# Performance work log

Measured on AMD Instinct MI355X. Metric: run time of the kernel, lower is better.

## Reference

```python
import jax, jax.numpy as jnp
import numpy as np

D = 512
H = 8
DV = D // H  # 64
NEG_INF = -1e30


def setup_inputs() -> dict:
    key = jax.random.key(0)
    ks = jax.random.split(key, 10)
    B, S = 4, 2048
    x = jax.random.normal(ks[0], (B, D, S), dtype=jnp.float32)
    mask = jnp.ones((B, S), dtype=jnp.float32)
    s = 1.0 / np.sqrt(D)
    sv = 1.0 / np.sqrt(D)
    # per-head Linear(d -> dv) weights stacked: [H, dv, d] (torch Linear layout W @ x)
    Wq = jax.random.uniform(ks[1], (H, DV, D), jnp.float32, -s, s)
    bq = jax.random.uniform(ks[2], (H, DV), jnp.float32, -s, s)
    Wk = jax.random.uniform(ks[3], (H, DV, D), jnp.float32, -s, s)
    bk = jax.random.uniform(ks[4], (H, DV), jnp.float32, -s, s)
    Wv = jax.random.uniform(ks[5], (H, DV, D), jnp.float32, -s, s)
    bv = jax.random.uniform(ks[6], (H, DV), jnp.float32, -s, s)
    W0 = jax.random.uniform(ks[7], (D, D), jnp.float32, -sv, sv)
    b0 = jax.random.uniform(ks[8], (D,), jnp.float32, -sv, sv)
    return {"x": x, "mask": mask, "Wq": Wq, "bq": bq, "Wk": Wk, "bk": bk,
            "Wv": Wv, "bv": bv, "W0": W0, "b0": b0}


def reference(x, mask, Wq, bq, Wk, bk, Wv, bv, W0, b0):
    # x: [B, d, S] -> xt: [B, S, d]
    xt = jnp.transpose(x, (0, 2, 1))
    # fused per-head projections: [B, H, S, dv]
    q = jnp.einsum('bsd,hed->bhse', xt, Wq) + bq[None, :, None, :]
    k = jnp.einsum('bsd,hed->bhse', xt, Wk) + bk[None, :, None, :]
    v = jnp.einsum('bsd,hed->bhse', xt, Wv) + bv[None, :, None, :]
    dv = q.shape[-1]
    scores = jnp.einsum('bhse,bhte->bhst', q, k) * (1.0 / np.sqrt(dv))
    # mask_logits (QANet style): keep where mask==1, else -1e30; mask over key dim
    h_mask = mask[:, None, None, :]  # [B,1,1,S]
    scores = scores * h_mask + (1.0 - h_mask) * NEG_INF
    p = jax.nn.softmax(scores, axis=-1)
    # zero out fully-masked query rows via v_mask on query dim
    p = p * mask[:, None, :, None]
    out = jnp.einsum('bhst,bhte->bhse', p, v)  # [B,H,S,dv]
    # concat heads along feature dim -> [B, S, d]
    B, _, S, _ = out.shape
    heads = jnp.transpose(out, (0, 2, 1, 3)).reshape(B, S, -1)
    y = heads @ W0.T + b0  # output projection
    return jnp.transpose(y, (0, 2, 1))  # [B, d, S]
```

## Files before the change

### kernel.cpp

```cpp
#include <hip/hip_runtime.h>

#define B_  4
#define D_  512
#define H_  8
#define DV_ 64
#define S_  2048

typedef __bf16 bf16;
typedef bf16  bf16x8 __attribute__((ext_vector_type(8)));
typedef bf16  bf16x4 __attribute__((ext_vector_type(4)));
typedef float f32x4  __attribute__((ext_vector_type(4)));

#define MFMA(a, b, c) __builtin_amdgcn_mfma_f32_16x16x32_bf16((a), (b), (c), 0, 0, 0)

#define GLOAD_LDS(g, l)                                                     \
    __builtin_amdgcn_global_load_lds(                                       \
        (const __attribute__((address_space(1))) void*)(g),                 \
        (__attribute__((address_space(3))) void*)(l), 16, 0, 0)

__global__ __launch_bounds__(256) void prep(
    const float* __restrict__ x, const float* __restrict__ Wq,
    const float* __restrict__ Wk, const float* __restrict__ Wv,
    const float* __restrict__ W0, bf16* __restrict__ xb, bf16* __restrict__ Wb) {
    const int bid = blockIdx.x;
    if (bid < 4096) {
        __shared__ float tile[32][33];
        const int sblk = bid % 64;
        const int dblk = (bid / 64) % 16;
        const int b    = bid / 1024;
        const int d0 = dblk * 32, s0 = sblk * 32;
        const int tx = threadIdx.x & 31;
        const int ty = threadIdx.x >> 5;
        const float* xp = x + (size_t)b * D_ * S_;
#pragma unroll
        for (int i = 0; i < 32; i += 8)
            tile[ty + i][tx] = xp[(size_t)(d0 + ty + i) * S_ + s0 + tx];
        __syncthreads();
        bf16* xbp = xb + ((size_t)b * S_ + s0) * D_ + d0;
#pragma unroll
        for (int i = 0; i < 32; i += 8)
            xbp[(size_t)(ty + i) * D_ + tx] = (bf16)tile[tx][ty + i];
    } else {
        const int f0 = ((bid - 4096) * 256 + threadIdx.x) * 16;
        const int src = f0 >> 18;
        const int off = f0 & 262143;
        const float* W = (src == 0) ? Wq : (src == 1) ? Wk : (src == 2) ? Wv : W0;
        float4 v0 = *(const float4*)&W[off];
        float4 v1 = *(const float4*)&W[off + 4];
        float4 v2 = *(const float4*)&W[off + 8];
        float4 v3 = *(const float4*)&W[off + 12];
        bf16x8 h0 = {(bf16)v0.x, (bf16)v0.y, (bf16)v0.z, (bf16)v0.w,
                     (bf16)v1.x, (bf16)v1.y, (bf16)v1.z, (bf16)v1.w};
        bf16x8 h1 = {(bf16)v2.x, (bf16)v2.y, (bf16)v2.z, (bf16)v2.w,
                     (bf16)v3.x, (bf16)v3.y, (bf16)v3.z, (bf16)v3.w};
        *(bf16x8*)&Wb[f0]     = h0;
        *(bf16x8*)&Wb[f0 + 8] = h1;
    }
}

__global__ __launch_bounds__(256) void gemm_qkv(
    const bf16* __restrict__ A, const bf16* __restrict__ Wb,
    const float* __restrict__ bq, const float* __restrict__ bk,
    const float* __restrict__ bv,
    bf16* __restrict__ Q, bf16* __restrict__ K, bf16* __restrict__ Vt) {
    __shared__ bf16 Asl[8192];
    __shared__ bf16 Bsl[8192];

    const int tid = threadIdx.x;
    const int w = tid >> 6, lane = tid & 63;
    const int m16 = lane & 15, quad = lane >> 4;
    const int wr = w & 1, wc = w >> 1;

    const int nblk = blockIdx.x % 12;
    const int mblk = blockIdx.x / 12;
    const int m0 = mblk * 128, n0 = nblk * 128;

    f32x4 acc[4][4];
#pragma unroll
    for (int i = 0; i < 4; ++i)
#pragma unroll
        for (int j = 0; j < 4; ++j) acc[i][j] = (f32x4){0.f, 0.f, 0.f, 0.f};

    for (int k0 = 0; k0 < D_; k0 += 64) {
        __syncthreads();
#pragma unroll
        for (int i = 0; i < 4; ++i) {
            const int c  = w * 4 + i;
            const int mt = c >> 1, kk = c & 1;
            const int row = mt * 16 + m16;
            const int col = k0 + kk * 32 + quad * 8;
            GLOAD_LDS(&A[(size_t)(m0 + row) * D_ + col],  &Asl[(c * 64 + lane) * 8]);
            GLOAD_LDS(&Wb[(size_t)(n0 + row) * D_ + col], &Bsl[(c * 64 + lane) * 8]);
        }
        __syncthreads();
#pragma unroll
        for (int kk = 0; kk < 2; ++kk) {
            bf16x8 af[4], bfv[4];
#pragma unroll
            for (int t = 0; t < 4; ++t) {
                af[t]  = *(const bf16x8*)&Asl[(((wr * 4 + t) * 2 + kk) * 64 + lane) * 8];
                bfv[t] = *(const bf16x8*)&Bsl[(((wc * 4 + t) * 2 + kk) * 64 + lane) * 8];
            }
#pragma unroll
            for (int mt = 0; mt < 4; ++mt)
#pragma unroll
                for (int nt = 0; nt < 4; ++nt)
                    acc[mt][nt] = MFMA(af[mt], bfv[nt], acc[mt][nt]);
        }
    }

    const int proj = n0 >> 9;
    const float* bias = (proj == 0) ? bq : (proj == 1) ? bk : bv;
#pragma unroll
    for (int mt = 0; mt < 4; ++mt)
#pragma unroll
        for (int nt = 0; nt < 4; ++nt) {
            const int nlin = n0 + wc * 64 + nt * 16 + m16;
            const int nr = nlin & 511;
            const int h = nr >> 6, e = nr & 63;
            const float bia = bias[nr];
            const int srow = m0 + wr * 64 + mt * 16 + quad * 4;
            const int b = srow >> 11, s = srow & 2047;
            if (proj == 2) {
                bf16x4 hv;
#pragma unroll
                for (int r = 0; r < 4; ++r) hv[r] = (bf16)(acc[mt][nt][r] + bia);
                *(bf16x4*)&Vt[(((size_t)b * H_ + h) * DV_ + e) * S_ + s] = hv;
            } else {
                bf16* dst = (proj == 0) ? Q : K;
#pragma unroll
                for (int r = 0; r < 4; ++r)
                    dst[(((size_t)b * H_ + h) * S_ + s + r) * DV_ + e] =
                        (bf16)(acc[mt][nt][r] + bia);
            }
        }
}

#define RS 36
__global__ __launch_bounds__(256, 2) void flash_attn(
    const bf16* __restrict__ Q, const bf16* __restrict__ K, const bf16* __restrict__ Vt,
    const float* __restrict__ mask, bf16* __restrict__ heads) {
    __shared__ union SMem {
        bf16 Ps[4][64][RS];
        struct { float O[64][65]; float L[64]; } red;
    } sm;

    const int bidx = blockIdx.x;
    const int qblk = bidx & 31;
    const int h    = (bidx >> 5) & 7;
    const int b    = bidx >> 8;
    const int q0   = qblk * 64;

    const int tid = threadIdx.x;
    const int w = tid >> 6, lane = tid & 63;
    const int m16 = lane & 15, quad = lane >> 4;

    const bf16* Qp = Q  + ((size_t)b * H_ + h) * S_ * DV_;
    const bf16* Kp = K  + ((size_t)b * H_ + h) * S_ * DV_;
    const bf16* Vp = Vt + ((size_t)b * H_ + h) * DV_ * S_;
    const float* mp = mask + (size_t)b * S_;

    bf16x8 qf[4][2];
#pragma unroll
    for (int mt = 0; mt < 4; ++mt)
#pragma unroll
        for (int kk = 0; kk < 2; ++kk) {
            bf16x8 v = *(const bf16x8*)&Qp[(size_t)(q0 + mt * 16 + m16) * DV_ +
                                           kk * 32 + quad * 8];
#pragma unroll
            for (int i = 0; i < 8; ++i) v[i] = (bf16)((float)v[i] * 0.125f);
            qf[mt][kk] = v;
        }

    bf16x8 ones;
#pragma unroll
    for (int i = 0; i < 8; ++i) ones[i] = (bf16)1.0f;

    f32x4 o[4][4];
    f32x4 lacc[4];
#pragma unroll
    for (int mt = 0; mt < 4; ++mt)
#pragma unroll
        for (int nt = 0; nt < 4; ++nt) o[mt][nt] = (f32x4){0.f, 0.f, 0.f, 0.f};
#pragma unroll
    for (int nt = 0; nt < 4; ++nt) lacc[nt] = (f32x4){0.f, 0.f, 0.f, 0.f};

    bf16x8 kfc[2][2], vfc[4];
    {
        const int tw = w * 32;
#pragma unroll
        for (int nt = 0; nt < 2; ++nt)
#pragma unroll
            for (int kk = 0; kk < 2; ++kk)
                kfc[nt][kk] = *(const bf16x8*)&Kp[(size_t)(tw + nt * 16 + m16) * DV_ +
                                                  kk * 32 + quad * 8];
#pragma unroll
        for (int mt = 0; mt < 4; ++mt)
            vfc[mt] = *(const bf16x8*)&Vp[(size_t)(mt * 16 + m16) * S_ + tw + quad * 8];
    }

    for (int t0 = 0; t0 < S_; t0 += 128) {
        const int tw = t0 + w * 32;
        const bool more = (t0 + 128) < S_;

        bf16x8 kfn[2][2], vfn[4];
        if (more) {
            const int twn = tw + 128;
#pragma unroll
            for (int nt = 0; nt < 2; ++nt)
#pragma unroll
                for (int kk = 0; kk < 2; ++kk)
                    kfn[nt][kk] = *(const bf16x8*)&Kp[(size_t)(twn + nt * 16 + m16) * DV_ +
                                                      kk * 32 + quad * 8];
#pragma unroll
            for (int mt = 0; mt < 4; ++mt)
                vfn[mt] = *(const bf16x8*)&Vp[(size_t)(mt * 16 + m16) * S_ + twn + quad * 8];
        }

        f32x4 sc[4][2];
#pragma unroll
        for (int mt = 0; mt < 4; ++mt)
#pragma unroll
            for (int nt = 0; nt < 2; ++nt) sc[mt][nt] = (f32x4){0.f, 0.f, 0.f, 0.f};
#pragma unroll
        for (int kk = 0; kk < 2; ++kk)
#pragma unroll
            for (int mt = 0; mt < 4; ++mt)
#pragma unroll
                for (int nt = 0; nt < 2; ++nt)
                    sc[mt][nt] = MFMA(qf[mt][kk], kfc[nt][kk], sc[mt][nt]);

        const float mk0 = mp[tw + m16],          mk1 = mp[tw + 16 + m16];
        const float ng0 = (1.0f - mk0) * -1e30f, ng1 = (1.0f - mk1) * -1e30f;
#pragma unroll
        for (int mt = 0; mt < 4; ++mt)
#pragma unroll
            for (int r = 0; r < 4; ++r) {
                const int row = mt * 16 + quad * 4 + r;
                sm.Ps[w][row][m16]      = (bf16)__expf(sc[mt][0][r] * mk0 + ng0);
                sm.Ps[w][row][16 + m16] = (bf16)__expf(sc[mt][1][r] * mk1 + ng1);
            }

        bf16x8 pf[4];
#pragma unroll
        for (int nt = 0; nt < 4; ++nt)
            pf[nt] = *(const bf16x8*)&sm.Ps[w][nt * 16 + m16][quad * 8];
#pragma unroll
        for (int mt = 0; mt < 4; ++mt)
#pragma unroll
            for (int nt = 0; nt < 4; ++nt) o[mt][nt] = MFMA(vfc[mt], pf[nt], o[mt][nt]);
#pragma unroll
        for (int nt = 0; nt < 4; ++nt) lacc[nt] = MFMA(ones, pf[nt], lacc[nt]);

        if (more) {
#pragma unroll
            for (int nt = 0; nt < 2; ++nt)
#pragma unroll
                for (int kk = 0; kk < 2; ++kk) kfc[nt][kk] = kfn[nt][kk];
#pragma unroll
            for (int mt = 0; mt < 4; ++mt) vfc[mt] = vfn[mt];
        }
    }

    __syncthreads();
#pragma unroll
    for (int ww = 0; ww < 4; ++ww) {
        if (w == ww) {
#pragma unroll
            for (int mt = 0; mt < 4; ++mt)
#pragma unroll
                for (int nt = 0; nt < 4; ++nt)
#pragma unroll
                    for (int r = 0; r < 4; ++r) {
                        float* slot = &sm.red.O[mt * 16 + quad * 4 + r][nt * 16 + m16];
                        *slot = (ww == 0) ? o[mt][nt][r] : (*slot + o[mt][nt][r]);
                    }
            if (quad == 0)
#pragma unroll
                for (int nt = 0; nt < 4; ++nt) {
                    float* ls = &sm.red.L[nt * 16 + m16];
                    *ls = (ww == 0) ? lacc[nt][0] : (*ls + lacc[nt][0]);
                }
        }
        __syncthreads();
    }

    const int ql = tid >> 2, ec = (tid & 3) * 16;
    const float l  = sm.red.L[ql];
    const float qm = mp[q0 + ql];
    const float inv = qm / l;
    bf16x8 hv[2];
#pragma unroll
    for (int c = 0; c < 2; ++c)
#pragma unroll
        for (int i = 0; i < 8; ++i)
            hv[c][i] = (bf16)(sm.red.O[ec + c * 8 + i][ql] * inv);
    bf16* dst = &heads[((size_t)b * S_ + q0 + ql) * D_ + h * DV_ + ec];
    *(bf16x8*)(dst)     = hv[0];
    *(bf16x8*)(dst + 8) = hv[1];
}

__global__ __launch_bounds__(256) void gemm_out(
    const bf16* __restrict__ A, const bf16* __restrict__ Wb,
    const float* __restrict__ b0, float* __restrict__ outp) {
    __shared__ bf16 Asl[8192];
    __shared__ bf16 Bsl[8192];

    const int tid = threadIdx.x;
    const int w = tid >> 6, lane = tid & 63;
    const int m16 = lane & 15, quad = lane >> 4;
    const int wr = w & 1, wc = w >> 1;

    const int nblk = blockIdx.x & 3;
    const int mblk = blockIdx.x >> 2;
    const int m0 = mblk * 128, n0 = nblk * 128;

    f32x4 acc[4][4];
#pragma unroll
    for (int i = 0; i < 4; ++i)
#pragma unroll
        for (int j = 0; j < 4; ++j) acc[i][j] = (f32x4){0.f, 0.f, 0.f, 0.f};

    for (int k0 = 0; k0 < D_; k0 += 64) {
        __syncthreads();
#pragma unroll
        for (int i = 0; i < 4; ++i) {
            const int c  = w * 4 + i;
            const int mt = c >> 1, kk = c & 1;
            const int row = mt * 16 + m16;
            const int col = k0 + kk * 32 + quad * 8;
            GLOAD_LDS(&A[(size_t)(m0 + row) * D_ + col], &Asl[(c * 64 + lane) * 8]);
            GLOAD_LDS(&Wb[(size_t)(1536 + n0 + row) * D_ + col], &Bsl[(c * 64 + lane) * 8]);
        }
        __syncthreads();
#pragma unroll
        for (int kk = 0; kk < 2; ++kk) {
            bf16x8 af[4], bfv[4];
#pragma unroll
            for (int t = 0; t < 4; ++t) {
                af[t]  = *(const bf16x8*)&Asl[(((wr * 4 + t) * 2 + kk) * 64 + lane) * 8];
                bfv[t] = *(const bf16x8*)&Bsl[(((wc * 4 + t) * 2 + kk) * 64 + lane) * 8];
            }
#pragma unroll
            for (int mt = 0; mt < 4; ++mt)
#pragma unroll
                for (int nt = 0; nt < 4; ++nt)
                    acc[mt][nt] = MFMA(af[mt], bfv[nt], acc[mt][nt]);
        }
    }

#pragma unroll
    for (int mt = 0; mt < 4; ++mt)
#pragma unroll
        for (int nt = 0; nt < 4; ++nt) {
            const int n = n0 + wc * 64 + nt * 16 + m16;
            const float bia = b0[n];
            const int srow = m0 + wr * 64 + mt * 16 + quad * 4;
            const int b = srow >> 11, s = srow & 2047;
            float4 vv;
            vv.x = acc[mt][nt][0] + bia;
            vv.y = acc[mt][nt][1] + bia;
            vv.z = acc[mt][nt][2] + bia;
            vv.w = acc[mt][nt][3] + bia;
            *(float4*)&outp[((size_t)b * D_ + n) * S_ + s] = vv;
        }
}

extern "C" void kernel_launch(void* const* d_in, const int* in_sizes, int n_in,
                              void* d_out, int out_size, void* d_ws, size_t ws_size,
                              hipStream_t stream) {
    const float* x    = (const float*)d_in[0];
    const float* mask = (const float*)d_in[1];
    const float* Wq   = (const float*)d_in[2];
    const float* bq   = (const float*)d_in[3];
    const float* Wk   = (const float*)d_in[4];
    const float* bk   = (const float*)d_in[5];
    const float* Wv   = (const float*)d_in[6];
    const float* bv   = (const float*)d_in[7];
    const float* W0   = (const float*)d_in[8];
    const float* b0   = (const float*)d_in[9];
    float* out = (float*)d_out;

    char* ws = (char*)d_ws;
    const size_t SEG = (size_t)B_ * S_ * D_ * sizeof(bf16);
    bf16* xb    = (bf16*)(ws);
    bf16* Qb    = (bf16*)(ws + SEG);
    bf16* Kb    = (bf16*)(ws + 2 * SEG);
    bf16* Vt    = (bf16*)(ws + 3 * SEG);
    bf16* Wb    = (bf16*)(ws + 4 * SEG);
    bf16* heads = xb;

    prep<<<dim3(4096 + 256), dim3(256), 0, stream>>>(x, Wq, Wk, Wv, W0, xb, Wb);
    gemm_qkv<<<dim3(64 * 12), dim3(256), 0, stream>>>(xb, Wb, bq, bk, bv, Qb, Kb, Vt);
    flash_attn<<<dim3(B_ * H_ * (S_ / 64)), dim3(256), 0, stream>>>(Qb, Kb, Vt, mask, heads);
    gemm_out<<<dim3(64 * 4), dim3(256), 0, stream>>>(heads, Wb, b0, out);
}
```

Before: 216.1 us.

## Compute transposed scores so P stays in registers, dropping LDS round-trip

Computes S^T = K·Q^T so each lane's MFMA accumulator already matches the B-operand layout needed for the P·V MFMA, removing the per-iteration LDS write and read of the probability tile. V fragments are gathered as two 4-element loads in a matching permuted key order, and the mask is loaded as vectors. The explicit register double-buffering of the next K/V tile is also removed, which frees registers but exposes global load latency unless the compiler or occupancy hides it.

```diff
diff --git a/kernel.cpp b/kernel.cpp
--- a/kernel.cpp
+++ b/kernel.cpp
@@ -136,14 +136,10 @@
         }
 }
 
-#define RS 36
 __global__ __launch_bounds__(256, 2) void flash_attn(
     const bf16* __restrict__ Q, const bf16* __restrict__ K, const bf16* __restrict__ Vt,
     const float* __restrict__ mask, bf16* __restrict__ heads) {
-    __shared__ union SMem {
-        bf16 Ps[4][64][RS];
-        struct { float O[64][65]; float L[64]; } red;
-    } sm;
+    __shared__ struct { float O[64][65]; float L[64]; } red;
 
     const int bidx = blockIdx.x;
     const int qblk = bidx & 31;
@@ -162,14 +158,14 @@
 
     bf16x8 qf[4][2];
 #pragma unroll
-    for (int mt = 0; mt < 4; ++mt)
+    for (int qt = 0; qt < 4; ++qt)
 #pragma unroll
         for (int kk = 0; kk < 2; ++kk) {
-            bf16x8 v = *(const bf16x8*)&Qp[(size_t)(q0 + mt * 16 + m16) * DV_ +
+            bf16x8 v = *(const bf16x8*)&Qp[(size_t)(q0 + qt * 16 + m16) * DV_ +
                                            kk * 32 + quad * 8];
 #pragma unroll
             for (int i = 0; i < 8; ++i) v[i] = (bf16)((float)v[i] * 0.125f);
-            qf[mt][kk] = v;
+            qf[qt][kk] = v;
         }
 
     bf16x8 ones;
@@ -181,85 +177,66 @@
 #pragma unroll
     for (int mt = 0; mt < 4; ++mt)
 #pragma unroll
-        for (int nt = 0; nt < 4; ++nt) o[mt][nt] = (f32x4){0.f, 0.f, 0.f, 0.f};
-#pragma unroll
-    for (int nt = 0; nt < 4; ++nt) lacc[nt] = (f32x4){0.f, 0.f, 0.f, 0.f};
-
-    bf16x8 kfc[2][2], vfc[4];
-    {
-        const int tw = w * 32;
-#pragma unroll
-        for (int nt = 0; nt < 2; ++nt)
-#pragma unroll
-            for (int kk = 0; kk < 2; ++kk)
-                kfc[nt][kk] = *(const bf16x8*)&Kp[(size_t)(tw + nt * 16 + m16) * DV_ +
-                                                  kk * 32 + quad * 8];
-#pragma unroll
-        for (int mt = 0; mt < 4; ++mt)
-            vfc[mt] = *(const bf16x8*)&Vp[(size_t)(mt * 16 + m16) * S_ + tw + quad * 8];
-    }
+        for (int qt = 0; qt < 4; ++qt) o[mt][qt] = (f32x4){0.f, 0.f, 0.f, 0.f};
+#pragma unroll
+    for (int qt = 0; qt < 4; ++qt) lacc[qt] = (f32x4){0.f, 0.f, 0.f, 0.f};
 
     for (int t0 = 0; t0 < S_; t0 += 128) {
         const int tw = t0 + w * 32;
-        const bool more = (t0 + 128) < S_;
-
-        bf16x8 kfn[2][2], vfn[4];
-        if (more) {
-            const int twn = tw + 128;
-#pragma unroll
-            for (int nt = 0; nt < 2; ++nt)
-#pragma unroll
-                for (int kk = 0; kk < 2; ++kk)
-                    kfn[nt][kk] = *(const bf16x8*)&Kp[(size_t)(twn + nt * 16 + m16) * DV_ +
-                                                      kk * 32 + quad * 8];
-#pragma unroll
-            for (int mt = 0; mt < 4; ++mt)
-                vfn[mt] = *(const bf16x8*)&Vp[(size_t)(mt * 16 + m16) * S_ + twn + quad * 8];
-        }
-
-        f32x4 sc[4][2];
+
+        bf16x8 kf[2][2];
+#pragma unroll
+        for (int tt = 0; tt < 2; ++tt)
+#pragma unroll
+            for (int kk = 0; kk < 2; ++kk)
+                kf[tt][kk] = *(const bf16x8*)&Kp[(size_t)(tw + tt * 16 + m16) * DV_ +
+                                                 kk * 32 + quad * 8];
+        bf16x8 vf[4];
+#pragma unroll
+        for (int mt = 0; mt < 4; ++mt) {
+            const bf16* vb = &Vp[(size_t)(mt * 16 + m16) * S_ + tw + quad * 4];
+            const bf16x4 lo = *(const bf16x4*)vb;
+            const bf16x4 hi = *(const bf16x4*)(vb + 16);
+#pragma unroll
+            for (int i = 0; i < 4; ++i) { vf[mt][i] = lo[i]; vf[mt][4 + i] = hi[i]; }
+        }
+        const f32x4 mq0 = *(const f32x4*)&mp[tw + quad * 4];
+        const f32x4 mq1 = *(const f32x4*)&mp[tw + 16 + quad * 4];
+
+        f32x4 sc[2][4];
+#pragma unroll
+        for (int tt = 0; tt < 2; ++tt)
+#pragma unroll
+            for (int qt = 0; qt < 4; ++qt) sc[tt][qt] = (f32x4){0.f, 0.f, 0.f, 0.f};
+#pragma unroll
+        for (int kk = 0; kk < 2; ++kk)
+#pragma unroll
+            for (int tt = 0; tt < 2; ++tt)
+#pragma unroll
+                for (int qt = 0; qt < 4; ++qt)
+                    sc[tt][qt] = MFMA(kf[tt][kk], qf[qt][kk], sc[tt][qt]);
+
+        f32x4 ng0, ng1;
+#pragma unroll
+        for (int r = 0; r < 4; ++r) {
+            ng0[r] = (1.0f - mq0[r]) * -1e30f;
+            ng1[r] = (1.0f - mq1[r]) * -1e30f;
+        }
+        bf16x8 pf[4];
+#pragma unroll
+        for (int qt = 0; qt < 4; ++qt)
+#pragma unroll
+            for (int r = 0; r < 4; ++r) {
+                pf[qt][r]     = (bf16)__expf(sc[0][qt][r] * mq0[r] + ng0[r]);
+                pf[qt][4 + r] = (bf16)__expf(sc[1][qt][r] * mq1[r] + ng1[r]);
+            }
+
 #pragma unroll
         for (int mt = 0; mt < 4; ++mt)
 #pragma unroll
-            for (int nt = 0; nt < 2; ++nt) sc[mt][nt] = (f32x4){0.f, 0.f, 0.f, 0.f};
-#pragma unroll
-        for (int kk = 0; kk < 2; ++kk)
-#pragma unroll
-            for (int mt = 0; mt < 4; ++mt)
-#pragma unroll
-                for (int nt = 0; nt < 2; ++nt)
-                    sc[mt][nt] = MFMA(qf[mt][kk], kfc[nt][kk], sc[mt][nt]);
-
-        const float mk0 = mp[tw + m16],          mk1 = mp[tw + 16 + m16];
-        const float ng0 = (1.0f - mk0) * -1e30f, ng1 = (1.0f - mk1) * -1e30f;
-#pragma unroll
-        for (int mt = 0; mt < 4; ++mt)
-#pragma unroll
-            for (int r = 0; r < 4; ++r) {
-                const int row = mt * 16 + quad * 4 + r;
-                sm.Ps[w][row][m16]      = (bf16)__expf(sc[mt][0][r] * mk0 + ng0);
-                sm.Ps[w][row][16 + m16] = (bf16)__expf(sc[mt][1][r] * mk1 + ng1);
-            }
-
-        bf16x8 pf[4];
-#pragma unroll
-        for (int nt = 0; nt < 4; ++nt)
-            pf[nt] = *(const bf16x8*)&sm.Ps[w][nt * 16 + m16][quad * 8];
-#pragma unroll
-        for (int mt = 0; mt < 4; ++mt)
-#pragma unroll
-            for (int nt = 0; nt < 4; ++nt) o[mt][nt] = MFMA(vfc[mt], pf[nt], o[mt][nt]);
-#pragma unroll
-        for (int nt = 0; nt < 4; ++nt) lacc[nt] = MFMA(ones, pf[nt], lacc[nt]);
-
-        if (more) {
-#pragma unroll
-            for (int nt = 0; nt < 2; ++nt)
-#pragma unroll
-                for (int kk = 0; kk < 2; ++kk) kfc[nt][kk] = kfn[nt][kk];
-#pragma unroll
-            for (int mt = 0; mt < 4; ++mt) vfc[mt] = vfn[mt];
-        }
+            for (int qt = 0; qt < 4; ++qt) o[mt][qt] = MFMA(vf[mt], pf[qt], o[mt][qt]);
+#pragma unroll
+        for (int qt = 0; qt < 4; ++qt) lacc[qt] = MFMA(ones, pf[qt], lacc[qt]);
     }
 
     __syncthreads();
@@ -269,24 +246,24 @@
 #pragma unroll
             for (int mt = 0; mt < 4; ++mt)
 #pragma unroll
-                for (int nt = 0; nt < 4; ++nt)
+                for (int qt = 0; qt < 4; ++qt)
 #pragma unroll
                     for (int r = 0; r < 4; ++r) {
-                        float* slot = &sm.red.O[mt * 16 + quad * 4 + r][nt * 16 + m16];
-                        *slot = (ww == 0) ? o[mt][nt][r] : (*slot + o[mt][nt][r]);
+                        float* slot = &red.O[mt * 16 + quad * 4 + r][qt * 16 + m16];
+                        *slot = (ww == 0) ? o[mt][qt][r] : (*slot + o[mt][qt][r]);
                     }
             if (quad == 0)
 #pragma unroll
-                for (int nt = 0; nt < 4; ++nt) {
-                    float* ls = &sm.red.L[nt * 16 + m16];
-                    *ls = (ww == 0) ? lacc[nt][0] : (*ls + lacc[nt][0]);
+                for (int qt = 0; qt < 4; ++qt) {
+                    float* ls = &red.L[qt * 16 + m16];
+                    *ls = (ww == 0) ? lacc[qt][0] : (*ls + lacc[qt][0]);
                 }
         }
         __syncthreads();
     }
 
     const int ql = tid >> 2, ec = (tid & 3) * 16;
-    const float l  = sm.red.L[ql];
+    const float l  = red.L[ql];
     const float qm = mp[q0 + ql];
     const float inv = qm / l;
     bf16x8 hv[2];
@@ -294,7 +271,7 @@
     for (int c = 0; c < 2; ++c)
 #pragma unroll
         for (int i = 0; i < 8; ++i)
-            hv[c][i] = (bf16)(sm.red.O[ec + c * 8 + i][ql] * inv);
+            hv[c][i] = (bf16)(red.O[ec + c * 8 + i][ql] * inv);
     bf16* dst = &heads[((size_t)b * S_ + q0 + ql) * D_ + h * DV_ + ec];
     *(bf16x8*)(dst)     = hv[0];
     *(bf16x8*)(dst + 8) = hv[1];
```

After: 239.9 us. +11.0%, slower.
